# Optimization experiments

Hardware: AMD Instinct MI355X
Metric: run time of the kernel (lower is better)

Reference implementation:

```python
import jax, jax.numpy as jnp
import numpy as np

IN_FEATURES = 4096
OUT_FEATURES = 16384


def setup_inputs() -> dict:
    key = jax.random.key(0)
    k_x, k_w, k_s, k_b = jax.random.split(key, 4)
    x = jax.random.normal(k_x, (2, 2048, IN_FEATURES), dtype=jnp.float32)
    # quantized weights take integer values in [-7, 7] like the triton kernel output
    weight_quantized = jax.random.randint(k_w, (OUT_FEATURES, IN_FEATURES), -7, 8, dtype=jnp.int32)
    # per-output-row scales (abs_max/7 style, strictly positive)
    weight_scale = jax.random.uniform(k_s, (OUT_FEATURES,), dtype=jnp.float32, minval=0.001, maxval=0.1)
    bias = jax.random.normal(k_b, (OUT_FEATURES,), dtype=jnp.float32) * 0.02
    return {"x": x, "weight_quantized": weight_quantized, "weight_scale": weight_scale, "bias": bias}


def reference(x, weight_quantized, weight_scale, bias):
    # dequantize: fp32 weight [out, in] = int8 weight * per-row scale
    weight = weight_quantized.astype(jnp.float32) * weight_scale[:, None]
    # F.linear: x @ weight.T + bias  -> [B, S, out]
    out = jnp.einsum('bsi,oi->bso', x, weight) + bias
    return out
```

## Files before the change

### kernel.cpp

```cpp
#include <hip/hip_runtime.h>
#include <stdint.h>

#define M_TOT 4096
#define K_DIM 4096
#define N_DIM 16384

typedef __attribute__((ext_vector_type(4))) int i32x4;

__device__ __forceinline__ int pack4(float a, float b, float c, float d, float inv) {
  int q0 = __float2int_rn(a * inv) & 255;
  int q1 = __float2int_rn(b * inv) & 255;
  int q2 = __float2int_rn(c * inv) & 255;
  int q3 = __float2int_rn(d * inv);
  return q0 | (q1 << 8) | (q2 << 16) | (q3 << 24);
}

__global__ __launch_bounds__(256)
void quant_x_k(const float* __restrict__ x, int4* __restrict__ xq,
               float* __restrict__ rowScale) {
  const int row = blockIdx.x;
  const int tid = threadIdx.x;
  const float* xr = x + (size_t)row * K_DIM + tid * 16;
  float4 v[4];
  float m = 0.f;
#pragma unroll
  for (int i = 0; i < 4; ++i) {
    v[i] = *(const float4*)(xr + i * 4);
    m = fmaxf(m, fmaxf(fmaxf(fabsf(v[i].x), fabsf(v[i].y)),
                       fmaxf(fabsf(v[i].z), fabsf(v[i].w))));
  }
#pragma unroll
  for (int off = 32; off > 0; off >>= 1)
    m = fmaxf(m, __shfl_xor(m, off));
  __shared__ float wmx[4];
  if ((tid & 63) == 0) wmx[tid >> 6] = m;
  __syncthreads();
  m = fmaxf(fmaxf(wmx[0], wmx[1]), fmaxf(wmx[2], wmx[3]));
  m = fmaxf(m, 1e-20f);
  if (tid == 0) rowScale[row] = m / 127.f;
  const float inv = 127.f / m;
  int4 o;
  o.x = pack4(v[0].x, v[0].y, v[0].z, v[0].w, inv);
  o.y = pack4(v[1].x, v[1].y, v[1].z, v[1].w, inv);
  o.z = pack4(v[2].x, v[2].y, v[2].z, v[2].w, inv);
  o.w = pack4(v[3].x, v[3].y, v[3].z, v[3].w, inv);
  xq[((size_t)row * K_DIM >> 4) + tid] = o;
}

__global__ void cvt_w_k(const int4* __restrict__ src, int4* __restrict__ dst, int n16) {
  int stride = gridDim.x * blockDim.x;
  for (int i = blockIdx.x * blockDim.x + threadIdx.x; i < n16; i += stride) {
    int4 o;
#pragma unroll
    for (int j = 0; j < 4; ++j) {
      int4 v = src[i * 4 + j];
      int p = (v.x & 255) | ((v.y & 255) << 8) | ((v.z & 255) << 16) | (v.w << 24);
      (&o.x)[j] = p;
    }
    dst[i] = o;
  }
}

__device__ __forceinline__ void gload16(const void* g, void* l) {
  __builtin_amdgcn_global_load_lds(
      (__attribute__((address_space(1))) void*)(g),
      (__attribute__((address_space(3))) void*)(l),
      16, 0, 0);
}

#define SWZ(o) ((o) ^ ((((o) >> 7) & 7) << 4))

#define MFMA_I8(a, b, c) __builtin_amdgcn_mfma_i32_16x16x64_i8(a, b, c, 0, 0, 0)

__global__ __launch_bounds__(512, 2)
void gemm_i8(const char* __restrict__ A, const char* __restrict__ W,
             const float* __restrict__ rowScale, const float* __restrict__ scale,
             const float* __restrict__ bias, float* __restrict__ C) {
  __shared__ __align__(16) char lds[131072];
  char* lbase = lds;

  const int tid  = threadIdx.x;
  const int lane = tid & 63;
  const int wave = tid >> 6;
  const int wm   = wave >> 2;
  const int wn   = wave & 3;
  const int r    = lane & 15;
  const int kq16 = (lane >> 4) << 4;

  const int nwg  = gridDim.x;
  const int bid  = blockIdx.x;
  const int wgid = (bid & 7) * (nwg >> 3) + (bid >> 3);
  const int tm   = wgid >> 6;
  const int tn   = wgid & 63;
  const int row0 = tm * 256;
  const int col0 = tn * 256;

  size_t tOff[4];
#pragma unroll
  for (int j = 0; j < 4; ++j) {
    int l = SWZ(j * 8192 + tid * 16);
    tOff[j] = (size_t)(l >> 7) * K_DIM + (l & 127);
  }
  const int tid16 = tid * 16;

  const char* Arow = A + (size_t)row0 * K_DIM;
  const char* Wrow = W + (size_t)col0 * K_DIM;

  i32x4 acc[8][4];
#pragma unroll
  for (int i = 0; i < 8; ++i)
#pragma unroll
    for (int j = 0; j < 4; ++j)
      acc[i][j] = (i32x4){0, 0, 0, 0};

#pragma unroll
  for (int j = 0; j < 4; ++j)
    gload16(Arow + tOff[j], lbase + j * 8192 + tid16);
#pragma unroll
  for (int j = 0; j < 4; ++j)
    gload16(Wrow + tOff[j], lbase + 32768 + j * 8192 + tid16);
  asm volatile("s_waitcnt vmcnt(0)" ::: "memory");
  __builtin_amdgcn_s_barrier();

  i32x4 a[4], b[4];

  for (int t = 0; t < 32; ++t) {
    const int curB = (t & 1) << 16;
    const int nxtB = curB ^ 65536;
    const int kb1  = ((t + 1 < 32) ? t + 1 : 31) * 128;

#pragma unroll
    for (int j = 0; j < 4; ++j)
      gload16(Arow + kb1 + tOff[j], lbase + nxtB + j * 8192 + tid16);
#pragma unroll
    for (int j = 0; j < 4; ++j)
      gload16(Wrow + kb1 + tOff[j], lbase + nxtB + 32768 + j * 8192 + tid16);

#pragma unroll
    for (int q = 0; q < 4; ++q)
      a[q] = *(const i32x4*)(lbase + curB + SWZ(((wm * 128 + q * 16 + r) << 7) + kq16));
#pragma unroll
    for (int q = 0; q < 4; ++q)
      b[q] = *(const i32x4*)(lbase + curB + 32768 + SWZ(((wn * 64 + q * 16 + r) << 7) + kq16));
    __builtin_amdgcn_s_setprio(1);
#pragma unroll
    for (int mi = 0; mi < 4; ++mi)
#pragma unroll
      for (int ni = 0; ni < 4; ++ni)
        acc[mi][ni] = MFMA_I8(a[mi], b[ni], acc[mi][ni]);
    __builtin_amdgcn_s_setprio(0);

#pragma unroll
    for (int q = 0; q < 4; ++q)
      a[q] = *(const i32x4*)(lbase + curB + SWZ(((wm * 128 + (4 + q) * 16 + r) << 7) + kq16));
    __builtin_amdgcn_s_setprio(1);
#pragma unroll
    for (int mi = 0; mi < 4; ++mi)
#pragma unroll
      for (int ni = 0; ni < 4; ++ni)
        acc[4 + mi][ni] = MFMA_I8(a[mi], b[ni], acc[4 + mi][ni]);
    __builtin_amdgcn_s_setprio(0);

#pragma unroll
    for (int q = 0; q < 4; ++q)
      a[q] = *(const i32x4*)(lbase + curB + SWZ(((wm * 128 + q * 16 + r) << 7) + 64 + kq16));
#pragma unroll
    for (int q = 0; q < 4; ++q)
      b[q] = *(const i32x4*)(lbase + curB + 32768 + SWZ(((wn * 64 + q * 16 + r) << 7) + 64 + kq16));
    __builtin_amdgcn_s_setprio(1);
#pragma unroll
    for (int mi = 0; mi < 4; ++mi)
#pragma unroll
      for (int ni = 0; ni < 4; ++ni)
        acc[mi][ni] = MFMA_I8(a[mi], b[ni], acc[mi][ni]);
    __builtin_amdgcn_s_setprio(0);

#pragma unroll
    for (int q = 0; q < 4; ++q)
      a[q] = *(const i32x4*)(lbase + curB + SWZ(((wm * 128 + (4 + q) * 16 + r) << 7) + 64 + kq16));
    __builtin_amdgcn_s_setprio(1);
#pragma unroll
    for (int mi = 0; mi < 4; ++mi)
#pragma unroll
      for (int ni = 0; ni < 4; ++ni)
        acc[4 + mi][ni] = MFMA_I8(a[mi], b[ni], acc[4 + mi][ni]);
    __builtin_amdgcn_s_setprio(0);

    asm volatile("s_waitcnt vmcnt(0)" ::: "memory");
    __builtin_amdgcn_s_barrier();
  }

  const int kq = kq16 >> 4;
  float rsv[8][4];
#pragma unroll
  for (int mi = 0; mi < 8; ++mi) {
    const int rowb = row0 + wm * 128 + mi * 16 + kq * 4;
#pragma unroll
    for (int q = 0; q < 4; ++q)
      rsv[mi][q] = rowScale[rowb + q];
  }
#pragma unroll
  for (int ni = 0; ni < 4; ++ni) {
    const int col = col0 + wn * 64 + ni * 16 + r;
    const float sc = scale[col];
    const float bv = bias[col];
#pragma unroll
    for (int mi = 0; mi < 8; ++mi) {
      const int rowb = row0 + wm * 128 + mi * 16 + kq * 4;
#pragma unroll
      for (int q = 0; q < 4; ++q)
        C[(size_t)(rowb + q) * N_DIM + col] =
            (float)acc[mi][ni][q] * (rsv[mi][q] * sc) + bv;
    }
  }
}

extern "C" void kernel_launch(void* const* d_in, const int* in_sizes, int n_in,
                              void* d_out, int out_size, void* d_ws, size_t ws_size,
                              hipStream_t stream) {
  const float* x      = (const float*)d_in[0];
  const int*   wq     = (const int*)d_in[1];
  const float* wscale = (const float*)d_in[2];
  const float* wbias  = (const float*)d_in[3];
  float* out = (float*)d_out;

  const size_t xq_bytes = (size_t)M_TOT * K_DIM;
  const size_t wq_bytes = (size_t)N_DIM * K_DIM;
  const size_t rs_bytes = (size_t)M_TOT * 4;
  if (ws_size < xq_bytes + wq_bytes + rs_bytes) return;

  char*  xq8 = (char*)d_ws;
  char*  wq8 = (char*)d_ws + xq_bytes;
  float* rs  = (float*)((char*)d_ws + xq_bytes + wq_bytes);

  quant_x_k<<<M_TOT, 256, 0, stream>>>(x, (int4*)xq8, rs);
  cvt_w_k<<<2048, 256, 0, stream>>>((const int4*)wq, (int4*)wq8,
                                    (N_DIM * K_DIM) / 16);

  const int grid = (M_TOT / 256) * (N_DIM / 256);
  gemm_i8<<<grid, 512, 0, stream>>>(xq8, wq8, rs, wscale, wbias, out);
}
```

Measured before the change: 381.7 us.

## Shrink GEMM tile to 128x256 with K-step 64 and 256 threads

Restructures the int8 GEMM to use 128x256 output tiles with 4 waves (2x2), a 64-byte K step and 48KB double-buffered LDS instead of 256x256 tiles with 8 waves and 128KB LDS. Each wave now computes 64x128 with 4x8 MFMA accumulators. The intent is higher occupancy (more blocks per CU) and twice as many workgroups, which improves latency hiding and load balance. The cost is lower arithmetic intensity per tile, more global traffic for W, and twice as many barrier iterations.

```diff
diff --git a/kernel.cpp b/kernel.cpp
--- a/kernel.cpp
+++ b/kernel.cpp
@@ -72,18 +72,18 @@
 
 #define MFMA_I8(a, b, c) __builtin_amdgcn_mfma_i32_16x16x64_i8(a, b, c, 0, 0, 0)
 
-__global__ __launch_bounds__(512, 2)
+__global__ __launch_bounds__(256, 2)
 void gemm_i8(const char* __restrict__ A, const char* __restrict__ W,
              const float* __restrict__ rowScale, const float* __restrict__ scale,
              const float* __restrict__ bias, float* __restrict__ C) {
-  __shared__ __align__(16) char lds[131072];
+  __shared__ __align__(16) char lds[49152];
   char* lbase = lds;
 
   const int tid  = threadIdx.x;
   const int lane = tid & 63;
   const int wave = tid >> 6;
-  const int wm   = wave >> 2;
-  const int wn   = wave & 3;
+  const int wm   = wave >> 1;
+  const int wn   = wave & 1;
   const int r    = lane & 15;
   const int kq16 = (lane >> 4) << 4;
 
@@ -92,121 +92,86 @@
   const int wgid = (bid & 7) * (nwg >> 3) + (bid >> 3);
   const int tm   = wgid >> 6;
   const int tn   = wgid & 63;
-  const int row0 = tm * 256;
+  const int row0 = tm * 128;
   const int col0 = tn * 256;
 
   size_t tOff[4];
 #pragma unroll
   for (int j = 0; j < 4; ++j) {
-    int l = SWZ(j * 8192 + tid * 16);
-    tOff[j] = (size_t)(l >> 7) * K_DIM + (l & 127);
-  }
-  const int tid16 = tid * 16;
+    int l = SWZ(j * 4096 + tid * 16);
+    tOff[j] = (size_t)(l >> 6) * K_DIM + (l & 63);
+  }
+  const int wbase = wave << 10;
 
   const char* Arow = A + (size_t)row0 * K_DIM;
   const char* Wrow = W + (size_t)col0 * K_DIM;
 
-  i32x4 acc[8][4];
-#pragma unroll
-  for (int i = 0; i < 8; ++i)
-#pragma unroll
-    for (int j = 0; j < 4; ++j)
+  i32x4 acc[4][8];
+#pragma unroll
+  for (int i = 0; i < 4; ++i)
+#pragma unroll
+    for (int j = 0; j < 8; ++j)
       acc[i][j] = (i32x4){0, 0, 0, 0};
 
 #pragma unroll
+  for (int j = 0; j < 2; ++j)
+    gload16(Arow + tOff[j], lbase + j * 4096 + wbase);
+#pragma unroll
   for (int j = 0; j < 4; ++j)
-    gload16(Arow + tOff[j], lbase + j * 8192 + tid16);
-#pragma unroll
-  for (int j = 0; j < 4; ++j)
-    gload16(Wrow + tOff[j], lbase + 32768 + j * 8192 + tid16);
+    gload16(Wrow + tOff[j], lbase + 8192 + j * 4096 + wbase);
   asm volatile("s_waitcnt vmcnt(0)" ::: "memory");
   __builtin_amdgcn_s_barrier();
 
-  i32x4 a[4], b[4];
-
-  for (int t = 0; t < 32; ++t) {
-    const int curB = (t & 1) << 16;
-    const int nxtB = curB ^ 65536;
-    const int kb1  = ((t + 1 < 32) ? t + 1 : 31) * 128;
-
+  i32x4 a[4], b[8];
+
+  for (int t = 0; t < 64; ++t) {
+    const int curB = (t & 1) ? 24576 : 0;
+    const int nxtB = curB ^ 24576;
+    const int kb1  = ((t + 1 < 64) ? t + 1 : 63) * 64;
+
+#pragma unroll
+    for (int j = 0; j < 2; ++j)
+      gload16(Arow + kb1 + tOff[j], lbase + nxtB + j * 4096 + wbase);
 #pragma unroll
     for (int j = 0; j < 4; ++j)
-      gload16(Arow + kb1 + tOff[j], lbase + nxtB + j * 8192 + tid16);
-#pragma unroll
-    for (int j = 0; j < 4; ++j)
-      gload16(Wrow + kb1 + tOff[j], lbase + nxtB + 32768 + j * 8192 + tid16);
+      gload16(Wrow + kb1 + tOff[j], lbase + nxtB + 8192 + j * 4096 + wbase);
 
 #pragma unroll
     for (int q = 0; q < 4; ++q)
-      a[q] = *(const i32x4*)(lbase + curB + SWZ(((wm * 128 + q * 16 + r) << 7) + kq16));
-#pragma unroll
-    for (int q = 0; q < 4; ++q)
-      b[q] = *(const i32x4*)(lbase + curB + 32768 + SWZ(((wn * 64 + q * 16 + r) << 7) + kq16));
+      a[q] = *(const i32x4*)(lbase + curB + SWZ(((wm * 64 + q * 16 + r) << 6) + kq16));
+#pragma unroll
+    for (int q = 0; q < 8; ++q)
+      b[q] = *(const i32x4*)(lbase + curB + 8192 +
+                             SWZ(((wn * 128 + q * 16 + r) << 6) + kq16));
     __builtin_amdgcn_s_setprio(1);
 #pragma unroll
     for (int mi = 0; mi < 4; ++mi)
 #pragma unroll
-      for (int ni = 0; ni < 4; ++ni)
+      for (int ni = 0; ni < 8; ++ni)
         acc[mi][ni] = MFMA_I8(a[mi], b[ni], acc[mi][ni]);
     __builtin_amdgcn_s_setprio(0);
 
-#pragma unroll
-    for (int q = 0; q < 4; ++q)
-      a[q] = *(const i32x4*)(lbase + curB + SWZ(((wm * 128 + (4 + q) * 16 + r) << 7) + kq16));
-    __builtin_amdgcn_s_setprio(1);
-#pragma unroll
-    for (int mi = 0; mi < 4; ++mi)
-#pragma unroll
-      for (int ni = 0; ni < 4; ++ni)
-        acc[4 + mi][ni] = MFMA_I8(a[mi], b[ni], acc[4 + mi][ni]);
-    __builtin_amdgcn_s_setprio(0);
-
-#pragma unroll
-    for (int q = 0; q < 4; ++q)
-      a[q] = *(const i32x4*)(lbase + curB + SWZ(((wm * 128 + q * 16 + r) << 7) + 64 + kq16));
-#pragma unroll
-    for (int q = 0; q < 4; ++q)
-      b[q] = *(const i32x4*)(lbase + curB + 32768 + SWZ(((wn * 64 + q * 16 + r) << 7) + 64 + kq16));
-    __builtin_amdgcn_s_setprio(1);
-#pragma unroll
-    for (int mi = 0; mi < 4; ++mi)
-#pragma unroll
-      for (int ni = 0; ni < 4; ++ni)
-        acc[mi][ni] = MFMA_I8(a[mi], b[ni], acc[mi][ni]);
-    __builtin_amdgcn_s_setprio(0);
-
-#pragma unroll
-    for (int q = 0; q < 4; ++q)
-      a[q] = *(const i32x4*)(lbase + curB + SWZ(((wm * 128 + (4 + q) * 16 + r) << 7) + 64 + kq16));
-    __builtin_amdgcn_s_setprio(1);
-#pragma unroll
-    for (int mi = 0; mi < 4; ++mi)
-#pragma unroll
-      for (int ni = 0; ni < 4; ++ni)
-        acc[4 + mi][ni] = MFMA_I8(a[mi], b[ni], acc[4 + mi][ni]);
-    __builtin_amdgcn_s_setprio(0);
-
     asm volatile("s_waitcnt vmcnt(0)" ::: "memory");
     __builtin_amdgcn_s_barrier();
   }
 
   const int kq = kq16 >> 4;
-  float rsv[8][4];
-#pragma unroll
-  for (int mi = 0; mi < 8; ++mi) {
-    const int rowb = row0 + wm * 128 + mi * 16 + kq * 4;
+  float rsv[4][4];
+#pragma unroll
+  for (int mi = 0; mi < 4; ++mi) {
+    const int rowb = row0 + wm * 64 + mi * 16 + kq * 4;
 #pragma unroll
     for (int q = 0; q < 4; ++q)
       rsv[mi][q] = rowScale[rowb + q];
   }
 #pragma unroll
-  for (int ni = 0; ni < 4; ++ni) {
-    const int col = col0 + wn * 64 + ni * 16 + r;
+  for (int ni = 0; ni < 8; ++ni) {
+    const int col = col0 + wn * 128 + ni * 16 + r;
     const float sc = scale[col];
     const float bv = bias[col];
 #pragma unroll
-    for (int mi = 0; mi < 8; ++mi) {
-      const int rowb = row0 + wm * 128 + mi * 16 + kq * 4;
+    for (int mi = 0; mi < 4; ++mi) {
+      const int rowb = row0 + wm * 64 + mi * 16 + kq * 4;
 #pragma unroll
       for (int q = 0; q < 4; ++q)
         C[(size_t)(rowb + q) * N_DIM + col] =
@@ -237,6 +202,6 @@
   cvt_w_k<<<2048, 256, 0, stream>>>((const int4*)wq, (int4*)wq8,
                                     (N_DIM * K_DIM) / 16);
 
-  const int grid = (M_TOT / 256) * (N_DIM / 256);
-  gemm_i8<<<grid, 512, 0, stream>>>(xq8, wq8, rs, wscale, wbias, out);
-}
+  const int grid = (M_TOT / 128) * (N_DIM / 256);
+  gemm_i8<<<grid, 256, 0, stream>>>(xq8, wq8, rs, wscale, wbias, out);
+}
```

Result: slower. 447.8 us (+17.3%).
